# Optimization experiments

Hardware: AMD Instinct MI355X
Metric: run time of the kernel (lower is better)

The kernel has to match this reference:

```python
import jax, jax.numpy as jnp
import numpy as np

TEMP = 0.05  # Trainer temp


def setup_inputs() -> dict:
    key = jax.random.key(0)
    k1, k2, k3 = jax.random.split(key, 3)
    B, C, D = 4096, 32768, 256
    x = jax.random.normal(k1, (B, D), dtype=jnp.float32)
    centrals = jax.random.normal(k2, (C, D), dtype=jnp.float32)
    # memory bank rows are kept unit-norm by the update rule
    centrals = centrals / jnp.linalg.norm(centrals, axis=1, keepdims=True)
    labels = jax.random.randint(k3, (B,), 0, C)
    return {"x": x, "centrals": centrals, "labels": labels}


def reference(x, centrals, labels):
    # new_f = F.normalize(model_out, dim=1)
    f = x / jnp.linalg.norm(x, axis=1, keepdims=True)          # [B, D]
    # CM.forward: inputs.mm(features.t()), then /= temp
    logits = (f @ centrals.T) / TEMP                           # [B, C]
    # ups = gather(exp(logits), labels); down = sum(exp(logits));  ups/down == softmax prob at label
    logp = jax.nn.log_softmax(logits, axis=1)
    p = jnp.exp(jnp.take_along_axis(logp, labels[:, None], axis=1)[:, 0])  # [B]
    return p
```

## Files before the change

kernel.cpp:

```cpp
#include <hip/hip_runtime.h>
#include <stdint.h>

typedef int i32x4 __attribute__((ext_vector_type(4)));
typedef int i32x8 __attribute__((ext_vector_type(8)));
typedef float f32x4 __attribute__((ext_vector_type(4)));

#define B_ROWS 4096
#define C_COLS 32768
#define D_DIM 256
#define LOG2E_OVER_TEMP 28.853900817779268f

#define BM 256
#define BC 64
#define CSPLIT 64
#define CPB (C_COLS / CSPLIT)
#define CTILES (CPB / BC)
#define NWAVES 4
#define TILE_BYTES (BC * D_DIM)
#define CVT_TILES (C_COLS / BC)

typedef __attribute__((address_space(3))) char lds_char_t;
typedef __attribute__((address_space(1))) const char glb_char_t;

__device__ __forceinline__ int pack4_fp8(float a, float b, float c, float d) {
  int r = 0;
  r = __builtin_amdgcn_cvt_pk_fp8_f32(a, b, r, false);
  r = __builtin_amdgcn_cvt_pk_fp8_f32(c, d, r, true);
  return r;
}

__global__ void prep_all(const float* __restrict__ x, const float* __restrict__ cent,
                         const int* __restrict__ labels, uint8_t* __restrict__ cq,
                         uint8_t* __restrict__ xq, float* __restrict__ elab) {
  int blk = blockIdx.x;
  if (blk < CVT_TILES) {
    int ct = blk;
    #pragma unroll
    for (int i = 0; i < 4; i++) {
      int slot = i * 256 + threadIdx.x;
      int col = slot & 63;
      int half = (slot >> 6) & 1;
      int kb = slot >> 7;
      int cc = ct * 64 + col;
      const float* src = cent + (size_t)cc * D_DIM + kb * 32 + half * 16;
      float4 v0 = ((const float4*)src)[0];
      float4 v1 = ((const float4*)src)[1];
      float4 v2 = ((const float4*)src)[2];
      float4 v3 = ((const float4*)src)[3];
      int4 o;
      o.x = pack4_fp8(v0.x, v0.y, v0.z, v0.w);
      o.y = pack4_fp8(v1.x, v1.y, v1.z, v1.w);
      o.z = pack4_fp8(v2.x, v2.y, v2.z, v2.w);
      o.w = pack4_fp8(v3.x, v3.y, v3.z, v3.w);
      *(int4*)(cq + (size_t)ct * TILE_BYTES + slot * 16) = o;
    }
  } else {
    int row = (blk - CVT_TILES) * (blockDim.x >> 6) + (threadIdx.x >> 6);
    int lane = threadIdx.x & 63;
    int lab = labels[row];
    const float4 xv = *(const float4*)(x + (size_t)row * D_DIM + lane * 4);
    const float4 cv = *(const float4*)(cent + (size_t)lab * D_DIM + lane * 4);
    float ss = xv.x * xv.x + xv.y * xv.y + xv.z * xv.z + xv.w * xv.w;
    float dc = xv.x * cv.x + xv.y * cv.y + xv.z * cv.z + xv.w * cv.w;
    #pragma unroll
    for (int m = 1; m < 64; m <<= 1) {
      ss += __shfl_xor(ss, m, 64);
      dc += __shfl_xor(dc, m, 64);
    }
    float inv = 1.0f / sqrtf(ss);
    float sc = inv * LOG2E_OVER_TEMP;
    *(int*)(xq + (size_t)row * D_DIM + lane * 4) =
        pack4_fp8(xv.x * sc, xv.y * sc, xv.z * sc, xv.w * sc);
    if (lane == 0) elab[row] = exp2f(dc * inv * LOG2E_OVER_TEMP);
  }
}

__device__ __forceinline__ void stage_tile(const uint8_t* __restrict__ src, char* buf,
                                           int w, int lane) {
  #pragma unroll
  for (int i = 0; i < 4; i++) {
    int slot_hi = i * NWAVES + w;
    __builtin_amdgcn_global_load_lds(
        (glb_char_t*)(const void*)(src + slot_hi * 1024 + lane * 16),
        (lds_char_t*)(void*)(buf + slot_hi * 1024), 16, 0, 0);
  }
}

__global__ void __launch_bounds__(256, 2)
gemm_expsum(const uint8_t* __restrict__ xq, const uint8_t* __restrict__ cq,
            float* __restrict__ partials) {
  __shared__ char Bs[2][TILE_BYTES];
  const int tid = threadIdx.x;
  const int w = tid >> 6, lane = tid & 63;
  const int fr = lane & 15, kq = lane >> 4;

  const int bid = blockIdx.x;
  const int xcd = bid & 7;
  const int j = bid >> 3;
  const int bx = j & 15;
  const int cs = xcd * 8 + (j >> 4);
  const int brow0 = bx * BM;
  const int tile0 = cs * CTILES;

  i32x8 a[4][2];
  #pragma unroll
  for (int rf = 0; rf < 4; rf++) {
    int row = brow0 + w * 64 + rf * 16 + fr;
    #pragma unroll
    for (int kh = 0; kh < 2; kh++)
      a[rf][kh] = *(const i32x8*)(xq + (size_t)row * D_DIM + kh * 128 + kq * 32);
  }

  float s[4][4] = {{0.f,0.f,0.f,0.f},{0.f,0.f,0.f,0.f},{0.f,0.f,0.f,0.f},{0.f,0.f,0.f,0.f}};
  const f32x4 vzero = {0.f, 0.f, 0.f, 0.f};

  stage_tile(cq + (size_t)tile0 * TILE_BYTES, Bs[0], w, lane);

  for (int t = 0; t < CTILES; t++) {
    __syncthreads();
    if (t + 1 < CTILES)
      stage_tile(cq + (size_t)(tile0 + t + 1) * TILE_BYTES, Bs[(t + 1) & 1], w, lane);

    const char* buf = Bs[t & 1];
    #pragma unroll
    for (int cf = 0; cf < 4; cf++) {
      const int col = cf * 16 + fr;
      i32x8 bf[2];
      #pragma unroll
      for (int kh = 0; kh < 2; kh++) {
        const int kb = kh * 4 + kq;
        const int off = kb * 2048 + col * 16;
        i32x4 lo = *(const i32x4*)(buf + off);
        i32x4 hi = *(const i32x4*)(buf + off + 1024);
        i32x8 b;
        #pragma unroll
        for (int q = 0; q < 4; q++) { b[q] = lo[q]; b[q + 4] = hi[q]; }
        bf[kh] = b;
      }
      f32x4 acc[4];
      #pragma unroll
      for (int rf = 0; rf < 4; rf++) {
        acc[rf] = __builtin_amdgcn_mfma_scale_f32_16x16x128_f8f6f4(
            a[rf][0], bf[0], vzero, 0, 0, 0, 0x7F7F7F7F, 0, 0x7F7F7F7F);
        acc[rf] = __builtin_amdgcn_mfma_scale_f32_16x16x128_f8f6f4(
            a[rf][1], bf[1], acc[rf], 0, 0, 0, 0x7F7F7F7F, 0, 0x7F7F7F7F);
      }
      #pragma unroll
      for (int rf = 0; rf < 4; rf++)
        #pragma unroll
        for (int r = 0; r < 4; r++)
          s[rf][r] += __builtin_amdgcn_exp2f(acc[rf][r]);
    }
  }

  #pragma unroll
  for (int rf = 0; rf < 4; rf++)
    #pragma unroll
    for (int r = 0; r < 4; r++) {
      float v = s[rf][r];
      v += __shfl_xor(v, 1, 64);
      v += __shfl_xor(v, 2, 64);
      v += __shfl_xor(v, 4, 64);
      v += __shfl_xor(v, 8, 64);
      s[rf][r] = v;
    }
  if (fr == 0) {
    int rowbase = brow0 + w * 64;
    #pragma unroll
    for (int rf = 0; rf < 4; rf++)
      #pragma unroll
      for (int r = 0; r < 4; r++)
        partials[(size_t)cs * B_ROWS + rowbase + rf * 16 + kq * 4 + r] = s[rf][r];
  }
}

__global__ void finalize(const float* __restrict__ partials, const float* __restrict__ elab,
                         float* __restrict__ out) {
  int b = blockIdx.x * blockDim.x + threadIdx.x;
  if (b >= B_ROWS) return;
  float ssum = 0.f;
  #pragma unroll
  for (int cs = 0; cs < CSPLIT; cs++) ssum += partials[(size_t)cs * B_ROWS + b];
  out[b] = elab[b] / ssum;
}

extern "C" void kernel_launch(void* const* d_in, const int* in_sizes, int n_in,
                              void* d_out, int out_size, void* d_ws, size_t ws_size,
                              hipStream_t stream) {
  const float* x = (const float*)d_in[0];
  const float* cent = (const float*)d_in[1];
  const int* labels = (const int*)d_in[2];
  float* out = (float*)d_out;

  char* ws = (char*)d_ws;
  uint8_t* xq = (uint8_t*)ws;
  uint8_t* cq = (uint8_t*)(ws + (size_t)B_ROWS * D_DIM);
  float* partials = (float*)(ws + (size_t)B_ROWS * D_DIM + (size_t)C_COLS * D_DIM);
  float* elab = partials + (size_t)CSPLIT * B_ROWS;

  prep_all<<<CVT_TILES + B_ROWS / 4, 256, 0, stream>>>(x, cent, labels, cq, xq, elab);
  gemm_expsum<<<dim3(B_ROWS / BM * CSPLIT), 256, 0, stream>>>(xq, cq, partials);
  finalize<<<B_ROWS / 256, 256, 0, stream>>>(partials, elab, out);
}
```

Measured before the change: 67.37 us.

## Load centroid fragments directly from global memory instead of LDS staging

```diff
diff --git a/kernel.cpp b/kernel.cpp
--- a/kernel.cpp
+++ b/kernel.cpp
@@ -15,12 +15,8 @@
 #define CSPLIT 64
 #define CPB (C_COLS / CSPLIT)
 #define CTILES (CPB / BC)
-#define NWAVES 4
 #define TILE_BYTES (BC * D_DIM)
 #define CVT_TILES (C_COLS / BC)
-
-typedef __attribute__((address_space(3))) char lds_char_t;
-typedef __attribute__((address_space(1))) const char glb_char_t;
 
 __device__ __forceinline__ int pack4_fp8(float a, float b, float c, float d) {
   int r = 0;
@@ -75,21 +71,9 @@
   }
 }
 
-__device__ __forceinline__ void stage_tile(const uint8_t* __restrict__ src, char* buf,
-                                           int w, int lane) {
-  #pragma unroll
-  for (int i = 0; i < 4; i++) {
-    int slot_hi = i * NWAVES + w;
-    __builtin_amdgcn_global_load_lds(
-        (glb_char_t*)(const void*)(src + slot_hi * 1024 + lane * 16),
-        (lds_char_t*)(void*)(buf + slot_hi * 1024), 16, 0, 0);
-  }
-}
-
 __global__ void __launch_bounds__(256, 2)
 gemm_expsum(const uint8_t* __restrict__ xq, const uint8_t* __restrict__ cq,
             float* __restrict__ partials) {
-  __shared__ char Bs[2][TILE_BYTES];
   const int tid = threadIdx.x;
   const int w = tid >> 6, lane = tid & 63;
   const int fr = lane & 15, kq = lane >> 4;
@@ -114,36 +98,30 @@
   float s[4][4] = {{0.f,0.f,0.f,0.f},{0.f,0.f,0.f,0.f},{0.f,0.f,0.f,0.f},{0.f,0.f,0.f,0.f}};
   const f32x4 vzero = {0.f, 0.f, 0.f, 0.f};
 
-  stage_tile(cq + (size_t)tile0 * TILE_BYTES, Bs[0], w, lane);
+  const uint8_t* bb = cq + (size_t)tile0 * TILE_BYTES + kq * 2048 + fr * 16;
 
+  #pragma unroll
   for (int t = 0; t < CTILES; t++) {
-    __syncthreads();
-    if (t + 1 < CTILES)
-      stage_tile(cq + (size_t)(tile0 + t + 1) * TILE_BYTES, Bs[(t + 1) & 1], w, lane);
-
-    const char* buf = Bs[t & 1];
     #pragma unroll
     for (int cf = 0; cf < 4; cf++) {
-      const int col = cf * 16 + fr;
-      i32x8 bf[2];
+      const uint8_t* p = bb + t * TILE_BYTES + cf * 256;
+      i32x4 lo0 = *(const i32x4*)(p);
+      i32x4 hi0 = *(const i32x4*)(p + 1024);
+      i32x4 lo1 = *(const i32x4*)(p + 8192);
+      i32x4 hi1 = *(const i32x4*)(p + 8192 + 1024);
+      i32x8 b0, b1;
       #pragma unroll
-      for (int kh = 0; kh < 2; kh++) {
-        const int kb = kh * 4 + kq;
-        const int off = kb * 2048 + col * 16;
-        i32x4 lo = *(const i32x4*)(buf + off);
-        i32x4 hi = *(const i32x4*)(buf + off + 1024);
-        i32x8 b;
-        #pragma unroll
-        for (int q = 0; q < 4; q++) { b[q] = lo[q]; b[q + 4] = hi[q]; }
-        bf[kh] = b;
+      for (int q = 0; q < 4; q++) {
+        b0[q] = lo0[q]; b0[q + 4] = hi0[q];
+        b1[q] = lo1[q]; b1[q + 4] = hi1[q];
       }
       f32x4 acc[4];
       #pragma unroll
       for (int rf = 0; rf < 4; rf++) {
         acc[rf] = __builtin_amdgcn_mfma_scale_f32_16x16x128_f8f6f4(
-            a[rf][0], bf[0], vzero, 0, 0, 0, 0x7F7F7F7F, 0, 0x7F7F7F7F);
+            a[rf][0], b0, vzero, 0, 0, 0, 0x7F7F7F7F, 0, 0x7F7F7F7F);
         acc[rf] = __builtin_amdgcn_mfma_scale_f32_16x16x128_f8f6f4(
-            a[rf][1], bf[1], acc[rf], 0, 0, 0, 0x7F7F7F7F, 0, 0x7F7F7F7F);
+            a[rf][1], b1, acc[rf], 0, 0, 0, 0x7F7F7F7F, 0, 0x7F7F7F7F);
       }
       #pragma unroll
       for (int rf = 0; rf < 4; rf++)
```

New measurement: 84.80 us. +25.9%, slower.
